# Performance work log

Hardware: AMD Instinct MI355X
Metric: run time of the kernel (lower is better)

## Reference

```python
import jax, jax.numpy as jnp
import numpy as np

WINDOW_SIZE = 11
SIGMA = 1.5
PAD = WINDOW_SIZE // 2

def _gaussian_window(ws=WINDOW_SIZE, sigma=SIGMA):
    x = jnp.arange(ws, dtype=jnp.float32) - ws // 2
    g = jnp.exp(-(x ** 2) / (2.0 * sigma ** 2))
    g = g / g.sum()
    w2d = jnp.outer(g, g)  # [ws, ws]
    return w2d[None, None, :, :]  # [O=1, I=1, ws, ws]

def _blur(x, w):
    # depthwise (channel=1) conv with SAME-style padding = ws//2
    return jax.lax.conv_general_dilated(
        x, w, window_strides=(1, 1), padding=[(PAD, PAD), (PAD, PAD)],
        dimension_numbers=('NCHW', 'OIHW', 'NCHW'))

def setup_inputs() -> dict:
    key = jax.random.key(0)
    k1, k2 = jax.random.split(key)
    pred = jax.random.uniform(k1, (32, 1, 512, 512), dtype=jnp.float32)
    target = jax.random.uniform(k2, (32, 1, 512, 512), dtype=jnp.float32)
    return {"pred": pred, "target": target}

def reference(pred, target):
    w = _gaussian_window().astype(pred.dtype)
    mu1 = _blur(pred, w)
    mu2 = _blur(target, w)
    mu1_sq = mu1 * mu1
    mu2_sq = mu2 * mu2
    mu1_mu2 = mu1 * mu2
    sigma1_sq = _blur(pred * pred, w) - mu1_sq
    sigma2_sq = _blur(target * target, w) - mu2_sq
    sigma12 = _blur(pred * target, w) - mu1_mu2
    C1 = 0.01 ** 2
    C2 = 0.03 ** 2
    ssim_map = ((2.0 * mu1_mu2 + C1) * (2.0 * sigma12 + C2)) / (
        (mu1_sq + mu2_sq + C1) * (sigma1_sq + sigma2_sq + C2))
    return 1.0 - ssim_map.mean()
```

## Files before the change

### kernel.cpp

```cpp
#include <hip/hip_runtime.h>
#include <hip/hip_bf16.h>


typedef float  f32x4  __attribute__((ext_vector_type(4)));
typedef short  short8 __attribute__((ext_vector_type(8)));
typedef short  short4v __attribute__((ext_vector_type(4)));

#define NBLOCK 512

__device__ __forceinline__ short bf16s(float x) {
    __hip_bfloat16 h = __float2bfloat16(x);
    return __builtin_bit_cast(short, h);
}
__device__ __forceinline__ float bf16f(float x) {
    unsigned u = (unsigned)__builtin_bit_cast(unsigned short,
                                              __float2bfloat16(x)) << 16;
    return __builtin_bit_cast(float, u);
}

__device__ __forceinline__ void gload16(const float* g, float* lds) {
    __builtin_amdgcn_global_load_lds(g, lds, 16, 0, 0);
}

#define WAITV4 asm volatile("s_waitcnt vmcnt(4)" ::: "memory")
#define WAITV0 asm volatile("s_waitcnt vmcnt(0)" ::: "memory")

__global__ __launch_bounds__(256, 2)
void ssim_main(const float* __restrict__ pred, const float* __restrict__ targ,
               float* __restrict__ partial) {
    const float W[11] = {
        0.00102840f, 0.00759876f, 0.03600077f, 0.10936070f, 0.21300554f,
        0.26601173f,
        0.21300554f, 0.10936070f, 0.03600077f, 0.00759876f, 0.00102840f};

    __shared__ __align__(16) short hring[4][4][16][72];
    __shared__ __align__(16) float rawbuf[4][2][1024];
    __shared__ float wsum[4];

    const int w     = threadIdx.x >> 6;
    const int L     = threadIdx.x & 63;
    const int n     = L & 15;
    const int quad  = L >> 4;
    const int waveId = blockIdx.x * 4 + w;
    const int img    = waveId >> 6;
    const int rem    = waveId & 63;
    const int q      = rem >> 5;
    const int stripe = rem & 31;
    const int c0     = stripe << 4;
    const int s0     = q << 4;
    const bool edge  = (stripe == 0) | (stripe == 31);

    const float* __restrict__ pim = pred + (size_t)img * 262144;
    const float* __restrict__ tim = targ + (size_t)img * 262144;

    float S = 0.f;
#pragma unroll
    for (int kk = 0; kk < 11; ++kk) S += bf16f(W[kk]);
    const float c2 = 1.0f / (S * S);

    short8 bw;
#pragma unroll
    for (int j = 0; j < 8; ++j) {
        const int d = quad * 8 + j - n - 3;
        bw[j] = bf16s((d >= 0 && d <= 10) ? W[d] : 0.f);
    }
    const f32x4 zc = {0.f, 0.f, 0.f, 0.f};

    const int  cb  = c0 - 8 + quad * 8;
    const int  cc0 = min(max(cb, 0), 508);
    const int  cc1 = min(max(cb + 4, 0), 508);
    const bool ok0 = (unsigned)cb < 512u;
    const bool ok1 = (unsigned)(cb + 4) < 512u;

    float lsum = 0.f;

    auto issue = [&](int Tt) {
        const int Tc = min(max(Tt, 0), 31);
        const int rowoff = ((Tc << 4) + n) * 512;
        float* sb = &rawbuf[w][Tt & 1][0];
        gload16(pim + rowoff + cc0, sb);
        gload16(pim + rowoff + cc1, sb + 256);
        gload16(tim + rowoff + cc0, sb + 512);
        gload16(tim + rowoff + cc1, sb + 768);
    };

    auto hproc = [&](int Tt) {
        const int wslot = (int)(((unsigned)(Tt << 4)) & 63u) + quad * 4;
        short4v o[4];
        if ((unsigned)Tt > 31u) {
#pragma unroll
            for (int f = 0; f < 4; ++f) o[f] = (short4v){0, 0, 0, 0};
        } else {
            const float* sb = &rawbuf[w][Tt & 1][0];
            f32x4 p0 = *(const f32x4*)(sb + (L << 2));
            f32x4 p1 = *(const f32x4*)(sb + 256 + (L << 2));
            f32x4 t0 = *(const f32x4*)(sb + 512 + (L << 2));
            f32x4 t1 = *(const f32x4*)(sb + 768 + (L << 2));
            if (edge) {
                p0 = ok0 ? p0 : zc;  p1 = ok1 ? p1 : zc;
                t0 = ok0 ? t0 : zc;  t1 = ok1 ? t1 : zc;
            }
            short8 fa[4];
#pragma unroll
            for (int j = 0; j < 4; ++j) {
                const float pj = p0[j], tj = t0[j];
                const float u = pj + tj, v = pj - tj;
                fa[0][j] = bf16s(pj);
                fa[1][j] = bf16s(tj);
                fa[2][j] = bf16s(u * u);
                fa[3][j] = bf16s(v * v);
            }
#pragma unroll
            for (int j = 0; j < 4; ++j) {
                const float pj = p1[j], tj = t1[j];
                const float u = pj + tj, v = pj - tj;
                fa[0][j + 4] = bf16s(pj);
                fa[1][j + 4] = bf16s(tj);
                fa[2][j + 4] = bf16s(u * u);
                fa[3][j + 4] = bf16s(v * v);
            }
#pragma unroll
            for (int f = 0; f < 4; ++f) {
                const f32x4 d = __builtin_amdgcn_mfma_f32_16x16x32_bf16(
                    fa[f], bw, zc, 0, 0, 0);
                short4v ov;
#pragma unroll
                for (int r2 = 0; r2 < 4; ++r2) ov[r2] = bf16s(d[r2]);
                o[f] = ov;
            }
        }
#pragma unroll
        for (int f = 0; f < 4; ++f)
            *(short4v*)&hring[w][f][n][wslot] = o[f];
    };

    auto vstep = [&](int s) {
        const int rslot0 = (int)(((unsigned)((s << 4) - 8)) & 63u);
        const int chunk  = (rslot0 + quad * 8) & 63;
        f32x4 dv[4];
#pragma unroll
        for (int f = 0; f < 4; ++f) {
            const short8 af = *(const short8*)&hring[w][f][n][chunk];
            dv[f] = __builtin_amdgcn_mfma_f32_16x16x32_bf16(af, bw, zc, 0, 0, 0);
        }
#pragma unroll
        for (int r = 0; r < 4; ++r) {
            const float m1 = dv[0][r] * c2, m2 = dv[1][r] * c2;
            const float Av = dv[2][r] * c2, Bv = dv[3][r] * c2;
            const float m12  = m1 * m2;
            const float smsq = m1 * m1 + m2 * m2;
            const float s12  = __builtin_fmaf(0.25f, Av - Bv, -m12);
            const float s1s2 = __builtin_fmaf(0.5f,  Av + Bv, -smsq);
            const float num = __builtin_fmaf(2.f, m12, 1e-4f) *
                              __builtin_fmaf(2.f, s12, 9e-4f);
            const float den = (smsq + 1e-4f) * (s1s2 + 9e-4f);
            float rc = __builtin_amdgcn_rcpf(den);
            rc = rc * (2.f - den * rc);
            lsum = __builtin_fmaf(num, rc, lsum);
        }
    };

    issue(s0 - 1); issue(s0);
    WAITV4; hproc(s0 - 1);
    issue(s0 + 1);
    WAITV4; hproc(s0);
    issue(s0 + 2);
    WAITV4; hproc(s0 + 1);
    issue(s0 + 3);

#pragma unroll 1
    for (int s = s0; s < s0 + 13; ++s) {
        vstep(s);
        WAITV4; hproc(s + 2);
        issue(s + 4);
    }
    vstep(s0 + 13); WAITV4; hproc(s0 + 15);
    vstep(s0 + 14); WAITV0; hproc(s0 + 16);
    vstep(s0 + 15);

#pragma unroll
    for (int off = 32; off > 0; off >>= 1)
        lsum += __shfl_down(lsum, off, 64);
    if (L == 0) wsum[w] = lsum;
    __syncthreads();
    if (threadIdx.x == 0)
        partial[blockIdx.x] = wsum[0] + wsum[1] + wsum[2] + wsum[3];
}

__global__ __launch_bounds__(128)
void ssim_finish(const float* __restrict__ partial, float* __restrict__ out) {
    __shared__ float ws2[2];
    const int t = threadIdx.x;
    const f32x4 v = *(const f32x4*)(partial + 4 * t);
    float s = v[0] + v[1] + v[2] + v[3];
#pragma unroll
    for (int off = 32; off > 0; off >>= 1)
        s += __shfl_down(s, off, 64);
    if ((t & 63) == 0) ws2[t >> 6] = s;
    __syncthreads();
    if (t == 0)
        out[0] = 1.0f - (ws2[0] + ws2[1]) * (1.0f / 8388608.0f);
}

extern "C" void kernel_launch(void* const* d_in, const int* in_sizes, int n_in,
                              void* d_out, int out_size, void* d_ws,
                              size_t ws_size, hipStream_t stream) {
    const float* pred = (const float*)d_in[0];
    const float* targ = (const float*)d_in[1];
    float* partial = (float*)d_ws;

    ssim_main<<<dim3(NBLOCK), dim3(256), 0, stream>>>(pred, targ, partial);
    ssim_finish<<<dim3(1), dim3(128), 0, stream>>>(partial, (float*)d_out);
    (void)in_sizes; (void)n_in; (void)out_size; (void)ws_size;
}
```

Before: 108.7 us.

## Replace LDS-staged async global loads with register double-buffered vector loads

Drops the global_load_lds staging buffer and manual vmcnt waits. Each tile's pred and target rows are now loaded straight into registers with two register sets (A/B) alternating, and the loop is unrolled by two to match. Launch bounds are raised to 4 blocks per CU, which freeing the LDS raw buffer allows, aiming at higher occupancy to hide latency. In exchange it adds register pressure from the extra buffered vectors and hands wait placement to the compiler.

```diff
diff --git a/kernel.cpp b/kernel.cpp
--- a/kernel.cpp
+++ b/kernel.cpp
@@ -18,14 +18,7 @@
     return __builtin_bit_cast(float, u);
 }
 
-__device__ __forceinline__ void gload16(const float* g, float* lds) {
-    __builtin_amdgcn_global_load_lds(g, lds, 16, 0, 0);
-}
-
-#define WAITV4 asm volatile("s_waitcnt vmcnt(4)" ::: "memory")
-#define WAITV0 asm volatile("s_waitcnt vmcnt(0)" ::: "memory")
-
-__global__ __launch_bounds__(256, 2)
+__global__ __launch_bounds__(256, 4)
 void ssim_main(const float* __restrict__ pred, const float* __restrict__ targ,
                float* __restrict__ partial) {
     const float W[11] = {
@@ -34,7 +27,6 @@
         0.21300554f, 0.10936070f, 0.03600077f, 0.00759876f, 0.00102840f};
 
     __shared__ __align__(16) short hring[4][4][16][72];
-    __shared__ __align__(16) float rawbuf[4][2][1024];
     __shared__ float wsum[4];
 
     const int w     = threadIdx.x >> 6;
@@ -74,65 +66,56 @@
 
     float lsum = 0.f;
 
-    auto issue = [&](int Tt) {
-        const int Tc = min(max(Tt, 0), 31);
-        const int rowoff = ((Tc << 4) + n) * 512;
-        float* sb = &rawbuf[w][Tt & 1][0];
-        gload16(pim + rowoff + cc0, sb);
-        gload16(pim + rowoff + cc1, sb + 256);
-        gload16(tim + rowoff + cc0, sb + 512);
-        gload16(tim + rowoff + cc1, sb + 768);
-    };
-
-    auto hproc = [&](int Tt) {
-        const int wslot = (int)(((unsigned)(Tt << 4)) & 63u) + quad * 4;
-        short4v o[4];
-        if ((unsigned)Tt > 31u) {
-#pragma unroll
-            for (int f = 0; f < 4; ++f) o[f] = (short4v){0, 0, 0, 0};
-        } else {
-            const float* sb = &rawbuf[w][Tt & 1][0];
-            f32x4 p0 = *(const f32x4*)(sb + (L << 2));
-            f32x4 p1 = *(const f32x4*)(sb + 256 + (L << 2));
-            f32x4 t0 = *(const f32x4*)(sb + 512 + (L << 2));
-            f32x4 t1 = *(const f32x4*)(sb + 768 + (L << 2));
-            if (edge) {
-                p0 = ok0 ? p0 : zc;  p1 = ok1 ? p1 : zc;
-                t0 = ok0 ? t0 : zc;  t1 = ok1 ? t1 : zc;
-            }
-            short8 fa[4];
-#pragma unroll
-            for (int j = 0; j < 4; ++j) {
-                const float pj = p0[j], tj = t0[j];
-                const float u = pj + tj, v = pj - tj;
-                fa[0][j] = bf16s(pj);
-                fa[1][j] = bf16s(tj);
-                fa[2][j] = bf16s(u * u);
-                fa[3][j] = bf16s(v * v);
-            }
-#pragma unroll
-            for (int j = 0; j < 4; ++j) {
-                const float pj = p1[j], tj = t1[j];
-                const float u = pj + tj, v = pj - tj;
-                fa[0][j + 4] = bf16s(pj);
-                fa[1][j + 4] = bf16s(tj);
-                fa[2][j + 4] = bf16s(u * u);
-                fa[3][j + 4] = bf16s(v * v);
-            }
-#pragma unroll
-            for (int f = 0; f < 4; ++f) {
-                const f32x4 d = __builtin_amdgcn_mfma_f32_16x16x32_bf16(
-                    fa[f], bw, zc, 0, 0, 0);
-                short4v ov;
-#pragma unroll
-                for (int r2 = 0; r2 < 4; ++r2) ov[r2] = bf16s(d[r2]);
-                o[f] = ov;
-            }
-        }
-#pragma unroll
-        for (int f = 0; f < 4; ++f)
-            *(short4v*)&hring[w][f][n][wslot] = o[f];
-    };
+#define LOADT(P0, P1, T0, T1, Tt)                                         \
+    {                                                                     \
+        const int Tc_ = min(max((Tt), 0), 31);                            \
+        const int ro_ = ((Tc_ << 4) + n) * 512;                           \
+        P0 = *(const f32x4*)(pim + ro_ + cc0);                            \
+        P1 = *(const f32x4*)(pim + ro_ + cc1);                            \
+        T0 = *(const f32x4*)(tim + ro_ + cc0);                            \
+        T1 = *(const f32x4*)(tim + ro_ + cc1);                            \
+    }
+
+#define HPROC(Tt, P0, P1, T0, T1)                                         \
+    {                                                                     \
+        const int wslot_ = (int)(((unsigned)((Tt) << 4)) & 63u) + quad*4; \
+        short4v o0_, o1_, o2_, o3_;                                       \
+        if ((unsigned)(Tt) > 31u) {                                       \
+            o0_ = (short4v){0,0,0,0}; o1_ = o0_; o2_ = o0_; o3_ = o0_;    \
+        } else {                                                          \
+            f32x4 p0_ = P0, p1_ = P1, t0_ = T0, t1_ = T1;                 \
+            if (edge) {                                                   \
+                p0_ = ok0 ? p0_ : zc;  p1_ = ok1 ? p1_ : zc;              \
+                t0_ = ok0 ? t0_ : zc;  t1_ = ok1 ? t1_ : zc;              \
+            }                                                             \
+            short8 fa0_, fa1_, fa2_, fa3_;                                \
+            _Pragma("unroll") for (int j = 0; j < 4; ++j) {               \
+                const float pj_ = p0_[j], tj_ = t0_[j];                   \
+                const float u_ = pj_ + tj_, v_ = pj_ - tj_;               \
+                fa0_[j] = bf16s(pj_);  fa1_[j] = bf16s(tj_);              \
+                fa2_[j] = bf16s(u_*u_); fa3_[j] = bf16s(v_*v_);           \
+            }                                                             \
+            _Pragma("unroll") for (int j = 0; j < 4; ++j) {               \
+                const float pj_ = p1_[j], tj_ = t1_[j];                   \
+                const float u_ = pj_ + tj_, v_ = pj_ - tj_;               \
+                fa0_[j+4] = bf16s(pj_);  fa1_[j+4] = bf16s(tj_);          \
+                fa2_[j+4] = bf16s(u_*u_); fa3_[j+4] = bf16s(v_*v_);       \
+            }                                                             \
+            f32x4 d_;                                                     \
+            d_ = __builtin_amdgcn_mfma_f32_16x16x32_bf16(fa0_,bw,zc,0,0,0);\
+            _Pragma("unroll") for (int r_=0;r_<4;++r_) o0_[r_]=bf16s(d_[r_]);\
+            d_ = __builtin_amdgcn_mfma_f32_16x16x32_bf16(fa1_,bw,zc,0,0,0);\
+            _Pragma("unroll") for (int r_=0;r_<4;++r_) o1_[r_]=bf16s(d_[r_]);\
+            d_ = __builtin_amdgcn_mfma_f32_16x16x32_bf16(fa2_,bw,zc,0,0,0);\
+            _Pragma("unroll") for (int r_=0;r_<4;++r_) o2_[r_]=bf16s(d_[r_]);\
+            d_ = __builtin_amdgcn_mfma_f32_16x16x32_bf16(fa3_,bw,zc,0,0,0);\
+            _Pragma("unroll") for (int r_=0;r_<4;++r_) o3_[r_]=bf16s(d_[r_]);\
+        }                                                                 \
+        *(short4v*)&hring[w][0][n][wslot_] = o0_;                         \
+        *(short4v*)&hring[w][1][n][wslot_] = o1_;                         \
+        *(short4v*)&hring[w][2][n][wslot_] = o2_;                         \
+        *(short4v*)&hring[w][3][n][wslot_] = o3_;                         \
+    }
 
     auto vstep = [&](int s) {
         const int rslot0 = (int)(((unsigned)((s << 4) - 8)) & 63u);
@@ -160,23 +143,29 @@
         }
     };
 
-    issue(s0 - 1); issue(s0);
-    WAITV4; hproc(s0 - 1);
-    issue(s0 + 1);
-    WAITV4; hproc(s0);
-    issue(s0 + 2);
-    WAITV4; hproc(s0 + 1);
-    issue(s0 + 3);
+    f32x4 AP0, AP1, AT0, AT1, BP0, BP1, BT0, BT1;
+
+    LOADT(AP0, AP1, AT0, AT1, s0 - 1)
+    LOADT(BP0, BP1, BT0, BT1, s0)
+    HPROC(s0 - 1, AP0, AP1, AT0, AT1)
+    LOADT(AP0, AP1, AT0, AT1, s0 + 1)
+    HPROC(s0, BP0, BP1, BT0, BT1)
+    LOADT(BP0, BP1, BT0, BT1, s0 + 2)
+    HPROC(s0 + 1, AP0, AP1, AT0, AT1)
+    LOADT(AP0, AP1, AT0, AT1, s0 + 3)
 
 #pragma unroll 1
-    for (int s = s0; s < s0 + 13; ++s) {
+    for (int i = 0; i < 8; ++i) {
+        const int s = s0 + 2 * i;
         vstep(s);
-        WAITV4; hproc(s + 2);
-        issue(s + 4);
-    }
-    vstep(s0 + 13); WAITV4; hproc(s0 + 15);
-    vstep(s0 + 14); WAITV0; hproc(s0 + 16);
-    vstep(s0 + 15);
+        HPROC(s + 2, BP0, BP1, BT0, BT1)
+        if (i < 7) LOADT(BP0, BP1, BT0, BT1, s + 4)
+        vstep(s + 1);
+        if (i < 7) {
+            HPROC(s + 3, AP0, AP1, AT0, AT1)
+            if (i < 6) LOADT(AP0, AP1, AT0, AT1, s + 5)
+        }
+    }
 
 #pragma unroll
     for (int off = 32; off > 0; off >>= 1)
@@ -185,6 +174,8 @@
     __syncthreads();
     if (threadIdx.x == 0)
         partial[blockIdx.x] = wsum[0] + wsum[1] + wsum[2] + wsum[3];
+#undef LOADT
+#undef HPROC
 }
 
 __global__ __launch_bounds__(128)
```

New measurement: 104.7 us. 3.7% less time.
